# Optimization experiments

Measured on AMD Instinct MI355X. Metric: run time of the kernel, lower is better.

The kernel has to match this reference:

```python
import jax, jax.numpy as jnp
import numpy as np

B, T, D_MODEL = 4, 4096, 512
HEADS, BUCKET_SIZE, N_HASHES = 8, 64, 4
DIM_HEAD = D_MODEL // HEADS  # 64
D_FFN = 2048
N_BUCKETS = T // BUCKET_SIZE  # 64
SELF_ATTN_VALUE = -5e4  # reformer TOKEN_SELF_ATTN_VALUE


def setup_inputs() -> dict:
    key = jax.random.key(0)
    ks = jax.random.split(key, 16)
    s = 0.02
    return {
        'x': jax.random.normal(ks[0], (B, T, D_MODEL), jnp.float32),
        'rotations': jax.random.normal(ks[1], (DIM_HEAD, N_HASHES, N_BUCKETS // 2), jnp.float32),
        'w_qk': jax.random.normal(ks[2], (D_MODEL, D_MODEL), jnp.float32) * s,
        'w_v': jax.random.normal(ks[3], (D_MODEL, D_MODEL), jnp.float32) * s,
        'w_out': jax.random.normal(ks[4], (D_MODEL, D_MODEL), jnp.float32) * s,
        'b_out': jnp.zeros((D_MODEL,), jnp.float32),
        'ln1_g': jnp.ones((D_MODEL,), jnp.float32),
        'ln1_b': jnp.zeros((D_MODEL,), jnp.float32),
        'w1': jax.random.normal(ks[5], (D_FFN, D_MODEL), jnp.float32) * s,
        'b1': jnp.zeros((D_FFN,), jnp.float32),
        'w2': jax.random.normal(ks[6], (D_MODEL, D_FFN), jnp.float32) * s,
        'b2': jnp.zeros((D_MODEL,), jnp.float32),
        'ln2_g': jnp.ones((D_MODEL,), jnp.float32),
        'ln2_b': jnp.zeros((D_MODEL,), jnp.float32),
    }


def layer_norm(x, g, b, eps=1e-6):
    m = x.mean(-1, keepdims=True)
    v = ((x - m) ** 2).mean(-1, keepdims=True)
    return (x - m) / jnp.sqrt(v + eps) * g + b


def look_one_back(x):
    # concat each chunk with the previous chunk (wrap-around), along in-chunk axis
    prev = jnp.roll(x, 1, axis=1)
    return jnp.concatenate([x, prev], axis=2)


def lsh_attention(qk, v, rotations):
    # qk, v: (bh, t, d) with shared-QK; rotations: (d, n_hashes, n_buckets//2)
    bh, t, d = qk.shape
    # --- hash: random rotations, argmax over [R, -R] ---
    rot = jnp.einsum('btf,fhi->bhti', qk, rotations)
    rot = jnp.concatenate([rot, -rot], axis=-1)        # (bh, H, t, n_buckets)
    buckets = jnp.argmax(rot, axis=-1)                 # (bh, H, t)
    buckets = buckets + (jnp.arange(N_HASHES) * N_BUCKETS)[None, :, None]
    buckets = buckets.reshape(bh, N_HASHES * t)
    # --- sort by (bucket, position) ---
    ticker = jnp.arange(N_HASHES * t)
    buckets_and_t = t * buckets + (ticker % t)[None, :]
    sticker = jnp.argsort(buckets_and_t, axis=-1)      # stable sort
    undo_sort = jnp.argsort(sticker, axis=-1)
    st = sticker % t                                   # original positions, sorted order
    sqk = jnp.take_along_axis(qk, st[..., None], axis=1)
    sv = jnp.take_along_axis(v, st[..., None], axis=1)
    # --- chunk: n_hashes*n_buckets chunks of bucket_size tokens ---
    n_chunks = N_HASHES * N_BUCKETS
    bq_t = st.reshape(bh, n_chunks, -1)
    bqk = sqk.reshape(bh, n_chunks, -1, d)
    bv = sv.reshape(bh, n_chunks, -1, d)
    bk = bqk / jnp.clip(jnp.linalg.norm(bqk, axis=-1, keepdims=True), 1e-6, None)
    bk = look_one_back(bk)
    bv = look_one_back(bv)
    bkv_t = look_one_back(bq_t)
    # --- local attention within chunk (+ previous chunk) ---
    dots = jnp.einsum('bcid,bcjd->bcij', bqk, bk) * (DIM_HEAD ** -0.5)
    self_mask = bq_t[..., None] == bkv_t[..., None, :]
    dots = jnp.where(self_mask, SELF_ATTN_VALUE, dots)
    logits = jax.nn.logsumexp(dots, axis=-1, keepdims=True)
    probs = jnp.exp(dots - logits)
    bo = jnp.einsum('bcij,bcjd->bcid', probs, bv)
    # --- unsort and combine hash rounds by softmax over round logits ---
    so = bo.reshape(bh, N_HASHES * t, d)
    slogits = logits.reshape(bh, N_HASHES * t)
    o = jnp.take_along_axis(so, undo_sort[..., None], axis=1).reshape(bh, N_HASHES, t, d)
    lg = jnp.take_along_axis(slogits, undo_sort, axis=1).reshape(bh, N_HASHES, t, 1)
    w = jnp.exp(lg - jax.nn.logsumexp(lg, axis=1, keepdims=True))
    return (o * w).sum(axis=1)                         # (bh, t, d)


def reference(x, rotations, w_qk, w_v, w_out, b_out, ln1_g, ln1_b, w1, b1, w2, b2, ln2_g, ln2_b):
    b, t, _ = x.shape
    qk = x @ w_qk.T
    v = x @ w_v.T

    def split_heads(u):
        return u.reshape(b, t, HEADS, DIM_HEAD).transpose(0, 2, 1, 3).reshape(b * HEADS, t, DIM_HEAD)

    attn = lsh_attention(split_heads(qk), split_heads(v), rotations)
    attn = attn.reshape(b, HEADS, t, DIM_HEAD).transpose(0, 2, 1, 3).reshape(b, t, D_MODEL)
    attn = attn @ w_out.T + b_out
    # residual + LN (dropout is identity at inference)
    h = layer_norm(attn + x, ln1_g, ln1_b)
    # position-wise FFN with its own residual + LN
    f = jax.nn.relu(h @ w1.T + b1) @ w2.T + b2
    return layer_norm(f + h, ln2_g, ln2_b)
```

## Files before the change

### kernel.cpp

```cpp
#include <hip/hip_runtime.h>
#include <stdint.h>

typedef unsigned short u16;
typedef __attribute__((ext_vector_type(4))) int   i32x4;
typedef __attribute__((ext_vector_type(4))) float f32x4;

__device__ __forceinline__ u16 f2bf(float x){
  unsigned int u = __float_as_uint(x);
  u += 0x7FFFu + ((u >> 16) & 1u);
  return (u16)(u >> 16);
}
__device__ __forceinline__ float bf2f(u16 h){
  return __uint_as_float(((unsigned int)h) << 16);
}
__device__ __forceinline__ unsigned int cvtpk_bf16(float lo, float hi){
  unsigned int r;
  asm("v_cvt_pk_bf16_f32 %0, %1, %2" : "=v"(r) : "v"(lo), "v"(hi));
  return r;
}
__device__ __forceinline__ f32x4 mfma16(i32x4 a, i32x4 b, f32x4 c){
  asm("v_mfma_f32_16x16x32_bf16 %0, %1, %2, %0" : "+v"(c) : "v"(a), "v"(b));
  return c;
}
__device__ __forceinline__ f32x4 acc_fence(f32x4 c){
  asm volatile("s_nop 7\ns_nop 7" : "+v"(c));
  return c;
}
__device__ __forceinline__ void gl_lds16(const void* g, void* l){
  unsigned long long ga = (unsigned long long)g;
  unsigned int la = (unsigned int)(unsigned long long)l;
  __builtin_amdgcn_global_load_lds((const __attribute__((address_space(1))) void*)ga,
                                   (__attribute__((address_space(3))) void*)la, 16, 0, 0);
}
__device__ __forceinline__ int xcd_swz(int f, int n){
  int chunk = n >> 3;
  return (f & 7) * chunk + (f >> 3);
}
__device__ __forceinline__ unsigned int f2mono(float v){
  unsigned int u = __float_as_uint(v);
  return u ^ ((unsigned int)((int)u >> 31) | 0x80000000u);
}
__device__ __forceinline__ float mono2f(unsigned int mu){
  unsigned int u = (mu & 0x80000000u) ? (mu ^ 0x80000000u) : ~mu;
  return __uint_as_float(u);
}
__device__ __forceinline__ unsigned long long shfl_xor_u64(unsigned long long x, int m){
  int lo = __shfl_xor((int)(unsigned int)(x & 0xFFFFFFFFull), m);
  int hi = __shfl_xor((int)(unsigned int)(x >> 32), m);
  return ((unsigned long long)(unsigned int)hi << 32) | (unsigned int)lo;
}

__global__ __launch_bounds__(256) void k_cvt(const float* __restrict__ in, u16* __restrict__ out, int n4){
  int i = blockIdx.x*256 + threadIdx.x;
  if (i >= n4) return;
  float4 v = ((const float4*)in)[i];
  ushort4 o; o.x=f2bf(v.x); o.y=f2bf(v.y); o.z=f2bf(v.z); o.w=f2bf(v.w);
  ((ushort4*)out)[i] = o;
}
__global__ __launch_bounds__(256) void k_split(const float* __restrict__ in, u16* __restrict__ hi, u16* __restrict__ lo, int n4){
  int i = blockIdx.x*256 + threadIdx.x;
  if (i >= n4) return;
  float4 v = ((const float4*)in)[i];
  ushort4 h, l;
  h.x=f2bf(v.x); l.x=f2bf(v.x - bf2f(h.x));
  h.y=f2bf(v.y); l.y=f2bf(v.y - bf2f(h.y));
  h.z=f2bf(v.z); l.z=f2bf(v.z - bf2f(h.z));
  h.w=f2bf(v.w); l.w=f2bf(v.w - bf2f(h.w));
  ((ushort4*)hi)[i]=h; ((ushort4*)lo)[i]=l;
}
__global__ __launch_bounds__(256) void k_rotT(const float* __restrict__ rot, u16* __restrict__ hi, u16* __restrict__ lo){
  int i = blockIdx.x*256 + threadIdx.x;
  if (i >= 8192) return;
  int d = i & 63, n = i >> 6;
  float v = rot[d*128 + n];
  u16 h = f2bf(v);
  hi[i] = h; lo[i] = f2bf(v - bf2f(h));
}

template<int MODE>
__global__ __launch_bounds__(256) void k_gemm(
    const u16* __restrict__ A0, const u16* __restrict__ B0,
    const float* __restrict__ bias,
    float* __restrict__ Cf, u16* __restrict__ Cb,
    int M, int N, int K)
{
  const int tid = threadIdx.x;
  const int l = tid & 63, w = tid >> 6;
  const int lr = l & 15, lg = l >> 4;
  int flat = blockIdx.y * gridDim.x + blockIdx.x;
  flat = xcd_swz(flat, gridDim.x * gridDim.y);
  const int m0 = (flat / gridDim.x) * 128, n0 = (flat % gridDim.x) * 128;
  const int mbase = (w >> 1) * 64, nbase = (w & 1) * 64;

  __shared__ __align__(16) u16 As[128*64];
  __shared__ __align__(16) u16 Bs[128*64];

  f32x4 zero = {0.f,0.f,0.f,0.f};
  f32x4 acc[4][4];
  #pragma unroll
  for (int i=0;i<4;i++)
    #pragma unroll
    for (int j=0;j<4;j++) acc[i][j] = zero;

  const int row_s = tid >> 3;
  const int c16   = tid & 7;

  for (int k0 = 0; k0 < K; k0 += 64){
    #pragma unroll
    for (int q=0;q<4;q++){
      int ra = q*32 + row_s;
      int cs = c16 ^ (ra & 7);
      gl_lds16(A0 + (size_t)(m0 + ra)*K + k0 + cs*8, (char*)As + q*4096 + tid*16);
      gl_lds16(B0 + (size_t)(n0 + ra)*K + k0 + cs*8, (char*)Bs + q*4096 + tid*16);
    }
    __syncthreads();
    #pragma unroll
    for (int kk=0; kk<64; kk+=32){
      i32x4 af[4], bfr[4];
      #pragma unroll
      for (int mf=0;mf<4;mf++){
        int row = mbase + mf*16 + lr;
        af[mf] = *(const i32x4*)((const char*)As + row*128 + (((kk*2) + (lg*16)) ^ ((row&7)<<4)));
      }
      #pragma unroll
      for (int nf=0;nf<4;nf++){
        int row = nbase + nf*16 + lr;
        bfr[nf] = *(const i32x4*)((const char*)Bs + row*128 + (((kk*2) + (lg*16)) ^ ((row&7)<<4)));
      }
      #pragma unroll
      for (int mf=0;mf<4;mf++)
        #pragma unroll
        for (int nf=0;nf<4;nf++)
          acc[mf][nf] = mfma16(af[mf], bfr[nf], acc[mf][nf]);
    }
    __syncthreads();
  }

  #pragma unroll
  for (int mf=0;mf<4;mf++){
    #pragma unroll
    for (int nf=0;nf<4;nf++){
      f32x4 v = acc_fence(acc[mf][nf]);
      #pragma unroll
      for (int r=0;r<4;r++){
        int m = m0 + mbase + mf*16 + lg*4 + r;
        int n = n0 + nbase + nf*16 + lr;
        float val = v[r];
        if (MODE == 0){
          if (bias) val += bias[n];
          Cf[(size_t)m*N + n] = val;
        } else if (MODE == 1){
          val += bias[n];
          val = fmaxf(val, 0.f);
          Cb[(size_t)m*N + n] = f2bf(val);
        } else {
          int b = m >> 12, t = m & 4095, h = n >> 6, d = n & 63;
          size_t idx = ((((size_t)(b*8 + h)) << 12) + t)*64 + d;
          Cb[idx] = f2bf(val);
        }
      }
    }
  }
}

__global__ __launch_bounds__(256) void k_gemmqk(
    const u16* __restrict__ Ah, const u16* __restrict__ Al,
    const u16* __restrict__ Bh, const u16* __restrict__ Bl,
    u16* __restrict__ qb, u16* __restrict__ qlo, u16* __restrict__ kn)
{
  const int K = 512;
  const int tid = threadIdx.x;
  const int l = tid & 63, w = tid >> 6;
  const int lr = l & 15, lg = l >> 4;
  int flat = blockIdx.y * gridDim.x + blockIdx.x;
  flat = xcd_swz(flat, gridDim.x * gridDim.y);
  const int m0 = (flat >> 2) * 128, n0 = (flat & 3) * 128;
  const int mbase = (w >> 1) * 64, nbase = (w & 1) * 64;

  __shared__ __align__(16) u16 AsH[128*64];
  __shared__ __align__(16) u16 AsL[128*64];
  __shared__ __align__(16) u16 BsH[128*64];
  __shared__ __align__(16) u16 BsL[128*64];

  f32x4 zero = {0.f,0.f,0.f,0.f};
  f32x4 acc[4][4];
  #pragma unroll
  for (int i=0;i<4;i++)
    #pragma unroll
    for (int j=0;j<4;j++) acc[i][j] = zero;

  const int row_s = tid >> 3;
  const int c16   = tid & 7;

  for (int k0 = 0; k0 < K; k0 += 64){
    #pragma unroll
    for (int q=0;q<4;q++){
      int ra = q*32 + row_s;
      int cs = c16 ^ (ra & 7);
      size_t ao = (size_t)(m0 + ra)*K + k0 + cs*8;
      size_t bo = (size_t)(n0 + ra)*K + k0 + cs*8;
      gl_lds16(Ah + ao, (char*)AsH + q*4096 + tid*16);
      gl_lds16(Al + ao, (char*)AsL + q*4096 + tid*16);
      gl_lds16(Bh + bo, (char*)BsH + q*4096 + tid*16);
      gl_lds16(Bl + bo, (char*)BsL + q*4096 + tid*16);
    }
    __syncthreads();
    #pragma unroll
    for (int kk=0; kk<64; kk+=32){
      i32x4 ah[4], al[4], bh2[4], bl2[4];
      #pragma unroll
      for (int mf=0;mf<4;mf++){
        int row = mbase + mf*16 + lr;
        int off = (((kk*2) + (lg*16)) ^ ((row&7)<<4));
        ah[mf] = *(const i32x4*)((const char*)AsH + row*128 + off);
        al[mf] = *(const i32x4*)((const char*)AsL + row*128 + off);
      }
      #pragma unroll
      for (int nf=0;nf<4;nf++){
        int row = nbase + nf*16 + lr;
        int off = (((kk*2) + (lg*16)) ^ ((row&7)<<4));
        bh2[nf] = *(const i32x4*)((const char*)BsH + row*128 + off);
        bl2[nf] = *(const i32x4*)((const char*)BsL + row*128 + off);
      }
      #pragma unroll
      for (int mf=0;mf<4;mf++)
        #pragma unroll
        for (int nf=0;nf<4;nf++){
          acc[mf][nf] = mfma16(ah[mf], bh2[nf], acc[mf][nf]);
          acc[mf][nf] = mfma16(al[mf], bh2[nf], acc[mf][nf]);
          acc[mf][nf] = mfma16(ah[mf], bl2[nf], acc[mf][nf]);
        }
    }
    __syncthreads();
  }

  const int hh = (n0 + nbase) >> 6;
  #pragma unroll
  for (int mf=0;mf<4;mf++){
    f32x4 v[4];
    #pragma unroll
    for (int nf=0;nf<4;nf++) v[nf] = acc_fence(acc[mf][nf]);
    #pragma unroll
    for (int r=0;r<4;r++){
      float ss = 0.f;
      #pragma unroll
      for (int nf=0;nf<4;nf++) ss += v[nf][r]*v[nf][r];
      ss += __shfl_xor(ss, 1); ss += __shfl_xor(ss, 2);
      ss += __shfl_xor(ss, 4); ss += __shfl_xor(ss, 8);
      float scale = 0.125f / fmaxf(sqrtf(ss), 1e-6f);
      int m = m0 + mbase + mf*16 + lg*4 + r;
      int b = m >> 12, t = m & 4095;
      size_t rowb = ((((size_t)(b*8 + hh)) << 12) + t) * 64;
      #pragma unroll
      for (int nf=0;nf<4;nf++){
        float val = v[nf][r];
        u16 hbf = f2bf(val);
        size_t idx = rowb + nf*16 + lr;
        qb [idx] = hbf;
        qlo[idx] = f2bf(val - bf2f(hbf));
        kn [idx] = f2bf(val * scale);
      }
    }
  }
}

__global__ __launch_bounds__(256) void k_hash2(
    const u16* __restrict__ qh, const u16* __restrict__ ql,
    const u16* __restrict__ rh, const u16* __restrict__ rl,
    int* __restrict__ bkt)
{
  const int tid = threadIdx.x;
  const int l = tid & 63, w = tid >> 6, lr = l & 15, lg = l >> 4;
  __shared__ __align__(16) u16 Rh[128*64];
  __shared__ __align__(16) u16 Rl[128*64];
  {
    const int row_s = tid >> 3, c8 = tid & 7;
    #pragma unroll
    for (int q = 0; q < 4; q++){
      int ra = q*32 + row_s;
      int cs = c8 ^ (ra & 7);
      gl_lds16(rh + ra*64 + cs*8, (char*)Rh + q*4096 + tid*16);
      gl_lds16(rl + ra*64 + cs*8, (char*)Rl + q*4096 + tid*16);
    }
  }
  const int blk = xcd_swz(blockIdx.x, gridDim.x);
  const int qrow = blk*64 + w*16 + lr;
  const size_t qoff = (size_t)qrow*64;
  i32x4 qhf[2], qlf[2];
  qhf[0] = *(const i32x4*)(qh + qoff + lg*8);
  qhf[1] = *(const i32x4*)(qh + qoff + 32 + lg*8);
  qlf[0] = *(const i32x4*)(ql + qoff + lg*8);
  qlf[1] = *(const i32x4*)(ql + qoff + 32 + lg*8);
  __syncthreads();

  f32x4 zero = {0.f,0.f,0.f,0.f};
  f32x4 acc[8];
  #pragma unroll
  for (int i=0;i<8;i++) acc[i] = zero;
  #pragma unroll
  for (int ks = 0; ks < 2; ks++){
    #pragma unroll
    for (int nf = 0; nf < 8; nf++){
      int row = nf*16 + lr;
      int off = (ks*64 + lg*16) ^ ((row & 7) << 4);
      i32x4 rhf = *(const i32x4*)((const char*)Rh + row*128 + off);
      i32x4 rlf = *(const i32x4*)((const char*)Rl + row*128 + off);
      acc[nf] = mfma16(rhf, qhf[ks], acc[nf]);
      acc[nf] = mfma16(rlf, qhf[ks], acc[nf]);
      acc[nf] = mfma16(rhf, qlf[ks], acc[nf]);
    }
  }

  const int bh = qrow >> 12, t = qrow & 4095;
  #pragma unroll
  for (int hh = 0; hh < 4; hh++){
    f32x4 v0 = acc_fence(acc[2*hh]);
    f32x4 v1 = acc_fence(acc[2*hh+1]);
    unsigned long long kmax = 0, kmin = 0;
    #pragma unroll
    for (int r = 0; r < 4; r++){
      int j0 = lg*4 + r, j1 = 16 + lg*4 + r;
      unsigned int mu0 = f2mono(v0[r]), mu1 = f2mono(v1[r]);
      unsigned long long a = ((unsigned long long)mu0 << 32) | (unsigned int)(31 - j0);
      unsigned long long b = ((unsigned long long)mu1 << 32) | (unsigned int)(31 - j1);
      if (a > kmax) kmax = a;
      if (b > kmax) kmax = b;
      unsigned long long c = ((unsigned long long)(~mu0) << 32) | (unsigned int)(31 - j0);
      unsigned long long d = ((unsigned long long)(~mu1) << 32) | (unsigned int)(31 - j1);
      if (c > kmin) kmin = c;
      if (d > kmin) kmin = d;
    }
    #pragma unroll
    for (int msk = 16; msk < 64; msk <<= 1){
      unsigned long long o1 = shfl_xor_u64(kmax, msk); if (o1 > kmax) kmax = o1;
      unsigned long long o2 = shfl_xor_u64(kmin, msk); if (o2 > kmin) kmin = o2;
    }
    if (lg == 0){
      float vmax = mono2f((unsigned int)(kmax >> 32));
      int jmax = 31 - (int)(kmax & 0xFFFFFFFFull);
      float vmin = mono2f(~(unsigned int)(kmin >> 32));
      int jmin = 31 - (int)(kmin & 0xFFFFFFFFull);
      int bucket = (vmax >= -vmin) ? jmax : 32 + jmin;
      bkt[((size_t)(bh*4 + hh) << 12) + t] = bucket;
    }
  }
}

__global__ __launch_bounds__(64) void k_sort(const int* __restrict__ buckets, int* __restrict__ st){
  const int grp = blockIdx.x;
  const int t = threadIdx.x;
  __shared__ int bkL[4096];
  __shared__ int hist[64][65];
  __shared__ int tot[64];
  const size_t gbase = ((size_t)grp) << 12;
  for (int i=0;i<64;i++)
    bkL[i*64 + t] = buckets[gbase + i*64 + t];
  #pragma unroll
  for (int b=0;b<64;b++) hist[t][b] = 0;
  __syncthreads();
  for (int i=0;i<64;i++){
    int b = bkL[t*64 + i];
    hist[t][b]++;
  }
  __syncthreads();
  { int run = 0;
    for (int tt=0; tt<64; tt++){ int v = hist[tt][t]; hist[tt][t] = run; run += v; }
    tot[t] = run; }
  __syncthreads();
  { int v = tot[t]; int incl = v;
    #pragma unroll
    for (int d=1; d<64; d<<=1){ int n = __shfl_up(incl, d, 64); if (t >= d) incl += n; }
    tot[t] = incl - v; }
  __syncthreads();
  const size_t obase = (((size_t)(grp>>2)) << 14) + ((size_t)(grp&3) << 12);
  for (int i=0;i<64;i++){
    int e = t*64 + i;
    int b = bkL[e];
    int dest = tot[b] + hist[t][b];
    hist[t][b]++;
    st[obase + dest] = e;
  }
}

__global__ __launch_bounds__(256, 4) void k_attn(
    const u16* __restrict__ qb, const u16* __restrict__ kn, const u16* __restrict__ vB,
    const int* __restrict__ st, float* __restrict__ lgt_out, u16* __restrict__ bo)
{
  int flat = blockIdx.y * gridDim.x + blockIdx.x;
  flat = xcd_swz(flat, gridDim.x * gridDim.y);
  const int c = flat & 255, bh = flat >> 8;
  const int rnd = c >> 6;
  const int tid = threadIdx.x;
  const int l = tid & 63, w = tid >> 6, lr = l & 15, lg = l >> 4;

  __shared__ __align__(16) u16 Ks[128*64];
  __shared__ __align__(16) u16 Vt[64][136];
  __shared__ int posk[128];

  if (tid < 128){
    int cc = (tid < 64) ? c : ((c + 255) & 255);
    posk[tid] = st[(((size_t)bh) << 14) + (cc << 6) + (tid & 63)];
  }
  __syncthreads();

  const size_t kvbase = ((size_t)bh) << 12;

  {
    const int rsub = l >> 3, c8 = l & 7;
    #pragma unroll
    for (int q2 = 0; q2 < 4; q2++){
      int row = w*32 + q2*8 + rsub;
      int cs = c8 ^ (row & 7);
      gl_lds16(kn + (kvbase + posk[row])*64 + cs*8,
               (char*)Ks + (w*4 + q2)*1024 + l*16);
    }
  }

  const int pos_q16 = posk[w*16 + lr];
  i32x4 qf[2];
  #pragma unroll
  for (int ks = 0; ks < 2; ks++)
    qf[ks] = *(const i32x4*)(qb + (kvbase + pos_q16)*64 + ks*32 + lg*8);

  {
    const int pp = tid & 63, db = tid >> 6;
    const int q5 = pp & 15;
    const int K0 = (pp >> 4)*32 + 16*((q5 >> 1) & 1) + 4*(q5 >> 2) + 2*(q5 & 1);
    const u16* r0 = vB + (kvbase + posk[K0])*64 + db*16;
    const u16* r1 = vB + (kvbase + posk[K0+1])*64 + db*16;
    uint4 a0 = *(const uint4*)r0, a1 = *(const uint4*)(r0 + 8);
    uint4 b0 = *(const uint4*)r1, b1 = *(const uint4*)(r1 + 8);
    uint av[8] = {a0.x,a0.y,a0.z,a0.w,a1.x,a1.y,a1.z,a1.w};
    uint bv[8] = {b0.x,b0.y,b0.z,b0.w,b1.x,b1.y,b1.z,b1.w};
    #pragma unroll
    for (int dd = 0; dd < 16; dd++){
      uint lo = (av[dd>>1] >> ((dd&1)*16)) & 0xFFFFu;
      uint hi = (bv[dd>>1] >> ((dd&1)*16)) & 0xFFFFu;
      *(uint*)((char*)&Vt[db*16 + dd][0] + pp*4) = lo | (hi << 16);
    }
  }
  __syncthreads();

  f32x4 zero = {0.f,0.f,0.f,0.f};
  f32x4 s[8];
  #pragma unroll
  for (int i=0;i<8;i++) s[i] = zero;
  __builtin_amdgcn_s_setprio(1);
  #pragma unroll
  for (int ks = 0; ks < 2; ks++){
    #pragma unroll
    for (int nf = 0; nf < 8; nf++){
      int row = nf*16 + lr;
      i32x4 kf = *(const i32x4*)((const char*)Ks + row*128 + ((ks*64 + lg*16) ^ ((row&7)<<4)));
      s[nf] = mfma16(kf, qf[ks], s[nf]);
    }
  }
  __builtin_amdgcn_s_setprio(0);

  float p[8][4];
  const int q_loc = w*16 + lr;
  float sum = 0.f;
  #pragma unroll
  for (int nf=0;nf<8;nf++){
    f32x4 t = acc_fence(s[nf]);
    #pragma unroll
    for (int r=0;r<4;r++){
      int k = nf*16 + lg*4 + r;
      float e = (k == q_loc) ? 0.f : __expf(t[r]);
      p[nf][r] = e;
      sum += e;
    }
  }
  sum += __shfl_xor(sum, 16);
  sum += __shfl_xor(sum, 32);
  float lv = logf(sum);
  float inv = 1.f / sum;
  if (l < 16)
    lgt_out[(((size_t)(bh*4 + rnd)) << 12) + pos_q16] = lv;

  i32x4 pa[4];
  #pragma unroll
  for (int ks=0;ks<4;ks++){
    uint w0 = cvtpk_bf16(p[2*ks][0],   p[2*ks][1]);
    uint w1 = cvtpk_bf16(p[2*ks][2],   p[2*ks][3]);
    uint w2 = cvtpk_bf16(p[2*ks+1][0], p[2*ks+1][1]);
    uint w3 = cvtpk_bf16(p[2*ks+1][2], p[2*ks+1][3]);
    i32x4 t = {(int)w0,(int)w1,(int)w2,(int)w3};
    pa[ks] = t;
  }

  f32x4 o[4];
  #pragma unroll
  for (int i=0;i<4;i++) o[i] = zero;
  __builtin_amdgcn_s_setprio(1);
  #pragma unroll
  for (int ks=0;ks<4;ks++){
    #pragma unroll
    for (int nf=0;nf<4;nf++){
      i32x4 vf = *(const i32x4*)((const char*)&Vt[nf*16 + lr][0] + ks*64 + lg*16);
      o[nf] = mfma16(pa[ks], vf, o[nf]);
    }
  }
  __builtin_amdgcn_s_setprio(0);
  float invq[4];
  #pragma unroll
  for (int r=0;r<4;r++) invq[r] = __shfl(inv, lg*4 + r, 64);
  #pragma unroll
  for (int nf=0;nf<4;nf++){
    f32x4 ov = acc_fence(o[nf]);
    #pragma unroll
    for (int r=0;r<4;r++){
      int q = w*16 + lg*4 + r;
      bo[((((size_t)(bh*4 + rnd)) << 12) + posk[q])*64 + nf*16 + lr] = f2bf(ov[r] * invq[r]);
    }
  }
}

__global__ __launch_bounds__(256) void k_combine(const u16* __restrict__ bo, const float* __restrict__ lgt,
                                                 u16* __restrict__ attn){
  const int wid = blockIdx.x * 4 + (threadIdx.x >> 6);
  const int l = threadIdx.x & 63;
  const int bh = wid >> 12, t = wid & 4095;
  const size_t lbase = (((size_t)bh) << 14) + t;
  float l0 = lgt[lbase], l1 = lgt[lbase + 4096], l2 = lgt[lbase + 8192], l3 = lgt[lbase + 12288];
  float m = fmaxf(fmaxf(l0,l1), fmaxf(l2,l3));
  float w0 = __expf(l0-m), w1 = __expf(l1-m), w2 = __expf(l2-m), w3 = __expf(l3-m);
  float inv = 1.f / (w0+w1+w2+w3);
  const size_t bbase = ((((size_t)bh) << 14) + t) * 64 + l;
  float o = w0 * bf2f(bo[bbase])
          + w1 * bf2f(bo[bbase + (size_t)4096*64])
          + w2 * bf2f(bo[bbase + (size_t)8192*64])
          + w3 * bf2f(bo[bbase + (size_t)12288*64]);
  o *= inv;
  int b = bh >> 3, h = bh & 7;
  attn[((((size_t)b) << 12) + t) * 512 + h*64 + l] = f2bf(o);
}

template<int WB16>
__global__ __launch_bounds__(256) void k_ln(const float* __restrict__ a, const float* __restrict__ res,
                                            const float* __restrict__ g, const float* __restrict__ bb,
                                            float* __restrict__ of, u16* __restrict__ ob){
  const int row = blockIdx.x*4 + (threadIdx.x >> 6);
  const int l = threadIdx.x & 63;
  const size_t base = (size_t)row*512 + l*8;
  float4 a0 = *(const float4*)(a + base);
  float4 a1 = *(const float4*)(a + base + 4);
  float4 r0 = *(const float4*)(res + base);
  float4 r1 = *(const float4*)(res + base + 4);
  float v[8] = {a0.x+r0.x, a0.y+r0.y, a0.z+r0.z, a0.w+r0.w,
                a1.x+r1.x, a1.y+r1.y, a1.z+r1.z, a1.w+r1.w};
  float sum = 0.f;
  #pragma unroll
  for (int j=0;j<8;j++) sum += v[j];
  #pragma unroll
  for (int msk=1; msk<64; msk<<=1) sum += __shfl_xor(sum, msk);
  float mean = sum * (1.f/512.f);
  float ss = 0.f;
  #pragma unroll
  for (int j=0;j<8;j++){ float d = v[j]-mean; ss += d*d; }
  #pragma unroll
  for (int msk=1; msk<64; msk<<=1) ss += __shfl_xor(ss, msk);
  float rstd = rsqrtf(ss * (1.f/512.f) + 1e-6f);
  float4 g0 = *(const float4*)(g + l*8),  g1 = *(const float4*)(g + l*8 + 4);
  float4 b0 = *(const float4*)(bb + l*8), b1 = *(const float4*)(bb + l*8 + 4);
  float gv[8] = {g0.x,g0.y,g0.z,g0.w,g1.x,g1.y,g1.z,g1.w};
  float bv[8] = {b0.x,b0.y,b0.z,b0.w,b1.x,b1.y,b1.z,b1.w};
  float y[8];
  #pragma unroll
  for (int j=0;j<8;j++) y[j] = (v[j]-mean)*rstd*gv[j] + bv[j];
  #pragma unroll
  for (int j=0;j<8;j++) of[base+j] = y[j];
  if (WB16){
    #pragma unroll
    for (int j=0;j<8;j++) ob[base+j] = f2bf(y[j]);
  }
}

extern "C" void kernel_launch(void* const* d_in, const int* in_sizes, int n_in,
                              void* d_out, int out_size, void* d_ws, size_t ws_size,
                              hipStream_t stream) {
  const float* x     = (const float*)d_in[0];
  const float* rot   = (const float*)d_in[1];
  const float* w_qk  = (const float*)d_in[2];
  const float* w_v   = (const float*)d_in[3];
  const float* w_out = (const float*)d_in[4];
  const float* b_out = (const float*)d_in[5];
  const float* ln1_g = (const float*)d_in[6];
  const float* ln1_b = (const float*)d_in[7];
  const float* w1    = (const float*)d_in[8];
  const float* b1    = (const float*)d_in[9];
  const float* w2    = (const float*)d_in[10];
  const float* b2    = (const float*)d_in[11];
  const float* ln2_g = (const float*)d_in[12];
  const float* ln2_b = (const float*)d_in[13];
  float* out = (float*)d_out;

  char* p = (char*)d_ws;
  u16*   xh   = (u16*)(p);
  u16*   xl   = (u16*)(p + 16777216);
  u16*   wqkh = (u16*)(p + 33554432);
  u16*   wqkl = (u16*)(p + 34078720);
  u16*   wvb  = (u16*)(p + 34603008);
  u16*   wob  = (u16*)(p + 35127296);
  u16*   w1b  = (u16*)(p + 35651584);
  u16*   w2b  = (u16*)(p + 37748736);
  u16*   qbuf = (u16*)(p + 39845888);
  u16*   knb  = (u16*)(p + 56623104);
  u16*   vb   = (u16*)(p + 73400320);
  int*   bkt  = (int*)(p + 90177536);
  int*   stb  = (int*)(p + 92274688);
  float* lgt  = (float*)(p + 94371840);
  u16*   bo   = (u16*)(p + 96468992);
  u16*   qlo   = bo;
  u16*   rothi = wqkh;
  u16*   rotlo = wqkl;
  u16*   attnc = xl;
  float* hf    = (float*)(p + 39845888);
  u16*   hb    = xh;
  u16*   hid   = bo;

  k_split<<<8192, 256, 0, stream>>>(x, xh, xl, 16384*512/4);
  k_split<<<256,  256, 0, stream>>>(w_qk, wqkh, wqkl, 512*512/4);
  k_cvt  <<<256,  256, 0, stream>>>(w_v,   wvb, 512*512/4);
  k_cvt  <<<256,  256, 0, stream>>>(w_out, wob, 512*512/4);
  k_cvt  <<<1024, 256, 0, stream>>>(w1, w1b, 2048*512/4);
  k_cvt  <<<1024, 256, 0, stream>>>(w2, w2b, 2048*512/4);

  k_gemmqk<<<dim3(4,128), 256, 0, stream>>>(xh, xl, wqkh, wqkl, qbuf, qlo, knb);
  k_gemm<3><<<dim3(4,128), 256, 0, stream>>>(xh, wvb, nullptr, nullptr, vb, 16384, 512, 512);
  k_rotT<<<32, 256, 0, stream>>>(rot, rothi, rotlo);
  k_hash2<<<2048, 256, 0, stream>>>(qbuf, qlo, rothi, rotlo, bkt);
  k_sort<<<128, 64, 0, stream>>>(bkt, stb);
  k_attn<<<dim3(256,32), 256, 0, stream>>>(qbuf, knb, vb, stb, lgt, bo);
  k_combine<<<32768, 256, 0, stream>>>(bo, lgt, attnc);
  k_gemm<0><<<dim3(4,128), 256, 0, stream>>>(attnc, wob, b_out, out, nullptr, 16384, 512, 512);
  k_ln<1><<<4096, 256, 0, stream>>>(out, x, ln1_g, ln1_b, hf, hb);
  k_gemm<1><<<dim3(16,128), 256, 0, stream>>>(hb, w1b, b1, nullptr, hid, 16384, 2048, 512);
  k_gemm<0><<<dim3(4,128), 256, 0, stream>>>(hid, w2b, b2, out, nullptr, 16384, 512, 2048);
  k_ln<0><<<4096, 256, 0, stream>>>(out, hf, ln2_g, ln2_b, out, nullptr);
}
```

Measured before the change: 315.0 us.

## Merge weight-prep launches, use exp2 in attention, drop fp32 LN1 output

Six weight-conversion launches and the rotation transpose are merged into one kernel with block-range dispatch, which cuts launch overhead. The attention softmax now uses the hardware exp2 with log2(e) folded into the key normalisation scale. Self-masking is rewritten to compare against a specific tile row, with an extra position check at chunk boundaries. LN1 no longer writes an fp32 copy, and LN2 reads the bf16 residual instead, which saves memory traffic but lowers residual precision, so the error against the reference may grow.

Result: faster. 300.1 us (-4.7%).

```diff
diff --git a/kernel.cpp b/kernel.cpp
--- a/kernel.cpp
+++ b/kernel.cpp
@@ -50,13 +50,6 @@
   return ((unsigned long long)(unsigned int)hi << 32) | (unsigned int)lo;
 }
 
-__global__ __launch_bounds__(256) void k_cvt(const float* __restrict__ in, u16* __restrict__ out, int n4){
-  int i = blockIdx.x*256 + threadIdx.x;
-  if (i >= n4) return;
-  float4 v = ((const float4*)in)[i];
-  ushort4 o; o.x=f2bf(v.x); o.y=f2bf(v.y); o.z=f2bf(v.z); o.w=f2bf(v.w);
-  ((ushort4*)out)[i] = o;
-}
 __global__ __launch_bounds__(256) void k_split(const float* __restrict__ in, u16* __restrict__ hi, u16* __restrict__ lo, int n4){
   int i = blockIdx.x*256 + threadIdx.x;
   if (i >= n4) return;
@@ -68,13 +61,44 @@
   h.w=f2bf(v.w); l.w=f2bf(v.w - bf2f(h.w));
   ((ushort4*)hi)[i]=h; ((ushort4*)lo)[i]=l;
 }
-__global__ __launch_bounds__(256) void k_rotT(const float* __restrict__ rot, u16* __restrict__ hi, u16* __restrict__ lo){
-  int i = blockIdx.x*256 + threadIdx.x;
-  if (i >= 8192) return;
-  int d = i & 63, n = i >> 6;
-  float v = rot[d*128 + n];
-  u16 h = f2bf(v);
-  hi[i] = h; lo[i] = f2bf(v - bf2f(h));
+
+__global__ __launch_bounds__(256) void k_wprep(
+    const float* __restrict__ w_qk, const float* __restrict__ w_v,
+    const float* __restrict__ w_out, const float* __restrict__ w1,
+    const float* __restrict__ w2, const float* __restrict__ rot,
+    u16* __restrict__ wqkh, u16* __restrict__ wqkl,
+    u16* __restrict__ wvb, u16* __restrict__ wob,
+    u16* __restrict__ w1b, u16* __restrict__ w2b,
+    u16* __restrict__ rothi, u16* __restrict__ rotlo)
+{
+  const int bid = blockIdx.x;
+  if (bid >= 2816){
+    int i = (bid - 2816)*256 + threadIdx.x;
+    int d = i & 63, n = i >> 6;
+    float v = rot[d*128 + n];
+    u16 h = f2bf(v);
+    rothi[i] = h; rotlo[i] = f2bf(v - bf2f(h));
+    return;
+  }
+  const int i = bid*256 + threadIdx.x;
+  if (i < 65536){
+    float4 v = ((const float4*)w_qk)[i];
+    ushort4 h, l;
+    h.x=f2bf(v.x); l.x=f2bf(v.x - bf2f(h.x));
+    h.y=f2bf(v.y); l.y=f2bf(v.y - bf2f(h.y));
+    h.z=f2bf(v.z); l.z=f2bf(v.z - bf2f(h.z));
+    h.w=f2bf(v.w); l.w=f2bf(v.w - bf2f(h.w));
+    ((ushort4*)wqkh)[i]=h; ((ushort4*)wqkl)[i]=l;
+    return;
+  }
+  const float* src; u16* dst; int j;
+  if (i < 131072){ src = w_v;  dst = wvb; j = i - 65536; }
+  else if (i < 196608){ src = w_out; dst = wob; j = i - 131072; }
+  else if (i < 458752){ src = w1;   dst = w1b; j = i - 196608; }
+  else { src = w2; dst = w2b; j = i - 458752; }
+  float4 v = ((const float4*)src)[j];
+  ushort4 o; o.x=f2bf(v.x); o.y=f2bf(v.y); o.z=f2bf(v.z); o.w=f2bf(v.w);
+  ((ushort4*)dst)[j] = o;
 }
 
 template<int MODE>
@@ -247,7 +271,7 @@
       for (int nf=0;nf<4;nf++) ss += v[nf][r]*v[nf][r];
       ss += __shfl_xor(ss, 1); ss += __shfl_xor(ss, 2);
       ss += __shfl_xor(ss, 4); ss += __shfl_xor(ss, 8);
-      float scale = 0.125f / fmaxf(sqrtf(ss), 1e-6f);
+      float scale = 0.18033688f / fmaxf(sqrtf(ss), 1e-6f);
       int m = m0 + mbase + mf*16 + lg*4 + r;
       int b = m >> 12, t = m & 4095;
       size_t rowb = ((((size_t)(b*8 + hh)) << 12) + t) * 64;
@@ -457,16 +481,17 @@
   }
   __builtin_amdgcn_s_setprio(0);
 
+  const bool bdry = (c & 63) == 0;
   float p[8][4];
-  const int q_loc = w*16 + lr;
   float sum = 0.f;
   #pragma unroll
   for (int nf=0;nf<8;nf++){
     f32x4 t = acc_fence(s[nf]);
     #pragma unroll
     for (int r=0;r<4;r++){
-      int k = nf*16 + lg*4 + r;
-      float e = (k == q_loc) ? 0.f : __expf(t[r]);
+      float e = __builtin_amdgcn_exp2f(t[r]);
+      if (nf == w && (lg*4 + r) == lr) e = 0.f;
+      if (nf >= 4 && bdry && posk[nf*16 + lg*4 + r] == pos_q16) e = 0.f;
       p[nf][r] = e;
       sum += e;
     }
@@ -537,7 +562,8 @@
 }
 
 template<int WB16>
-__global__ __launch_bounds__(256) void k_ln(const float* __restrict__ a, const float* __restrict__ res,
+__global__ __launch_bounds__(256) void k_ln(const float* __restrict__ a,
+                                            const float* __restrict__ resf, const u16* __restrict__ resb,
                                             const float* __restrict__ g, const float* __restrict__ bb,
                                             float* __restrict__ of, u16* __restrict__ ob){
   const int row = blockIdx.x*4 + (threadIdx.x >> 6);
@@ -545,10 +571,23 @@
   const size_t base = (size_t)row*512 + l*8;
   float4 a0 = *(const float4*)(a + base);
   float4 a1 = *(const float4*)(a + base + 4);
-  float4 r0 = *(const float4*)(res + base);
-  float4 r1 = *(const float4*)(res + base + 4);
-  float v[8] = {a0.x+r0.x, a0.y+r0.y, a0.z+r0.z, a0.w+r0.w,
-                a1.x+r1.x, a1.y+r1.y, a1.z+r1.z, a1.w+r1.w};
+  float rv[8];
+  if (WB16){
+    float4 r0 = *(const float4*)(resf + base);
+    float4 r1 = *(const float4*)(resf + base + 4);
+    rv[0]=r0.x; rv[1]=r0.y; rv[2]=r0.z; rv[3]=r0.w;
+    rv[4]=r1.x; rv[5]=r1.y; rv[6]=r1.z; rv[7]=r1.w;
+  } else {
+    uint4 rr = *(const uint4*)(resb + base);
+    uint rw[4] = {rr.x, rr.y, rr.z, rr.w};
+    #pragma unroll
+    for (int j=0;j<4;j++){
+      rv[2*j]   = bf2f((u16)(rw[j] & 0xFFFF));
+      rv[2*j+1] = bf2f((u16)(rw[j] >> 16));
+    }
+  }
+  float v[8] = {a0.x+rv[0], a0.y+rv[1], a0.z+rv[2], a0.w+rv[3],
+                a1.x+rv[4], a1.y+rv[5], a1.z+rv[6], a1.w+rv[7]};
   float sum = 0.f;
   #pragma unroll
   for (int j=0;j<8;j++) sum += v[j];
@@ -568,11 +607,12 @@
   float y[8];
   #pragma unroll
   for (int j=0;j<8;j++) y[j] = (v[j]-mean)*rstd*gv[j] + bv[j];
-  #pragma unroll
-  for (int j=0;j<8;j++) of[base+j] = y[j];
   if (WB16){
     #pragma unroll
     for (int j=0;j<8;j++) ob[base+j] = f2bf(y[j]);
+  } else {
+    #pragma unroll
+    for (int j=0;j<8;j++) of[base+j] = y[j];
   }
 }
 
@@ -612,30 +652,24 @@
   float* lgt  = (float*)(p + 94371840);
   u16*   bo   = (u16*)(p + 96468992);
   u16*   qlo   = bo;
-  u16*   rothi = wqkh;
-  u16*   rotlo = wqkl;
+  u16*   rothi = (u16*)(p + 96468992 + 16777216);
+  u16*   rotlo = (u16*)(p + 96468992 + 16777216 + 16384);
   u16*   attnc = xl;
-  float* hf    = (float*)(p + 39845888);
   u16*   hb    = xh;
   u16*   hid   = bo;
 
   k_split<<<8192, 256, 0, stream>>>(x, xh, xl, 16384*512/4);
-  k_split<<<256,  256, 0, stream>>>(w_qk, wqkh, wqkl, 512*512/4);
-  k_cvt  <<<256,  256, 0, stream>>>(w_v,   wvb, 512*512/4);
-  k_cvt  <<<256,  256, 0, stream>>>(w_out, wob, 512*512/4);
-  k_cvt  <<<1024, 256, 0, stream>>>(w1, w1b, 2048*512/4);
-  k_cvt  <<<1024, 256, 0, stream>>>(w2, w2b, 2048*512/4);
-
+  k_wprep<<<2848, 256, 0, stream>>>(w_qk, w_v, w_out, w1, w2, rot,
+                                    wqkh, wqkl, wvb, wob, w1b, w2b, rothi, rotlo);
   k_gemmqk<<<dim3(4,128), 256, 0, stream>>>(xh, xl, wqkh, wqkl, qbuf, qlo, knb);
   k_gemm<3><<<dim3(4,128), 256, 0, stream>>>(xh, wvb, nullptr, nullptr, vb, 16384, 512, 512);
-  k_rotT<<<32, 256, 0, stream>>>(rot, rothi, rotlo);
   k_hash2<<<2048, 256, 0, stream>>>(qbuf, qlo, rothi, rotlo, bkt);
   k_sort<<<128, 64, 0, stream>>>(bkt, stb);
   k_attn<<<dim3(256,32), 256, 0, stream>>>(qbuf, knb, vb, stb, lgt, bo);
   k_combine<<<32768, 256, 0, stream>>>(bo, lgt, attnc);
   k_gemm<0><<<dim3(4,128), 256, 0, stream>>>(attnc, wob, b_out, out, nullptr, 16384, 512, 512);
-  k_ln<1><<<4096, 256, 0, stream>>>(out, x, ln1_g, ln1_b, hf, hb);
+  k_ln<1><<<4096, 256, 0, stream>>>(out, x, nullptr, ln1_g, ln1_b, nullptr, hb);
   k_gemm<1><<<dim3(16,128), 256, 0, stream>>>(hb, w1b, b1, nullptr, hid, 16384, 2048, 512);
   k_gemm<0><<<dim3(4,128), 256, 0, stream>>>(hid, w2b, b2, out, nullptr, 16384, 512, 2048);
-  k_ln<0><<<4096, 256, 0, stream>>>(out, hf, ln2_g, ln2_b, out, nullptr);
-}
+  k_ln<0><<<4096, 256, 0, stream>>>(out, nullptr, hb, ln2_g, ln2_b, out, nullptr);
+}
```
